# Performance work log

Measured on AMD Instinct MI355X. Metric: run time of the kernel, lower is better.

The kernel has to match this reference:

```python
import jax, jax.numpy as jnp
import numpy as np

K_CURV = 1.0   # Lorentz(k=1.0)
EPS = 1e-6


def _project(space):
    # lift space components onto hyperboloid: t = sqrt(k + ||s||^2)
    t = jnp.sqrt(K_CURV + jnp.sum(space * space, axis=-1, keepdims=True))
    return jnp.concatenate([t, space], axis=-1)


def setup_inputs():
    key = jax.random.key(0)
    B, N, D, H = 4, 1024, 128, 8
    ks = jax.random.split(key, 7)
    # valid Lorentz points: [B, N, D] with x[...,0] the time coordinate
    x = _project(jax.random.normal(ks[0], (B, N, D - 1), dtype=jnp.float32) * 0.5)
    scale = 1.0 / np.sqrt(D)
    Wq = jax.random.normal(ks[1], (H, D - 1, D), dtype=jnp.float32) * scale
    Wk = jax.random.normal(ks[2], (H, D - 1, D), dtype=jnp.float32) * scale
    Wv = jax.random.normal(ks[3], (H, D - 1, D), dtype=jnp.float32) * scale
    bq = jnp.zeros((H, D - 1), dtype=jnp.float32)
    bk = jnp.zeros((H, D - 1), dtype=jnp.float32)
    bv = jnp.zeros((H, D - 1), dtype=jnp.float32)
    beta = jnp.ones((H,), dtype=jnp.float32)
    gamma = jnp.zeros((H,), dtype=jnp.float32)
    return {"x": x, "Wq": Wq, "bq": bq, "Wk": Wk, "bk": bk, "Wv": Wv, "bv": bv,
            "beta": beta, "gamma": gamma}


def _lorentz_fc(x, W, b):
    # HyboNet-style Lorentz fully-connected (identity activation), all heads at once.
    # x: [B,N,D], W: [H,D-1,D], b: [H,D-1] -> [H,B,N,D] on the hyperboloid
    space = jnp.einsum('bnd,hed->hbne', x, W) + b[:, None, None, :]
    return _project(space)


def reference(x, Wq, bq, Wk, bk, Wv, bv, beta, gamma):
    D = x.shape[-1]
    sign = jnp.concatenate([-jnp.ones((1,), x.dtype), jnp.ones((D - 1,), x.dtype)])
    Q = _lorentz_fc(x, Wq, bq)   # [H,B,N,D]
    K = _lorentz_fc(x, Wk, bk)
    V = _lorentz_fc(x, Wv, bv)
    # pairwise Minkowski inner product <q,k>_L = -t_q t_k + s_q . s_k
    inner = jnp.einsum('hbid,hbjd->hbij', Q * sign, K)          # [H,B,N,N]
    dists = jnp.arccosh(jnp.maximum(-inner / K_CURV, 1.0 + EPS)) * np.sqrt(K_CURV)
    scores = -beta[:, None, None, None] * dists - gamma[:, None, None, None]
    attn = jax.nn.softmax(scores, axis=-1)
    # Lorentz midpoint: normalize weighted sum back onto the hyperboloid
    mid = jnp.einsum('hbij,hbjd->hbid', attn, V)                # [H,B,N,D]
    mnorm = jnp.einsum('hbid,hbid->hbi', mid * sign, mid)       # <m,m>_L (negative)
    head_out = mid * (np.sqrt(K_CURV) / jnp.sqrt(jnp.maximum(-mnorm, EPS)))[..., None]
    # direct_concat: concatenate space parts, recompute time coordinate
    H = head_out.shape[0]
    t = head_out[..., 0]                                        # [H,B,N]
    s = jnp.moveaxis(head_out[..., 1:], 0, 2)                   # [B,N,H,D-1]
    space_cat = s.reshape(s.shape[0], s.shape[1], -1)           # [B,N,H*(D-1)]
    time = jnp.sqrt(jnp.maximum(jnp.sum(t * t, axis=0) - (H - 1) * K_CURV, EPS))
    return jnp.concatenate([time[..., None], space_cat], axis=-1)  # [B,N,H*(D-1)+1]
```

## Files before the change

### kernel.cpp

```cpp
#include <hip/hip_runtime.h>

typedef __attribute__((ext_vector_type(8))) short short8_t;
typedef __attribute__((ext_vector_type(4))) short short4_t;
typedef __attribute__((ext_vector_type(4))) float float4_t;
typedef __attribute__((ext_vector_type(2))) unsigned int uint2_t;

__device__ __forceinline__ unsigned short f2bf(float f) {
    unsigned u = __builtin_bit_cast(unsigned, f);
    u += 0x7FFFu + ((u >> 16) & 1u);
    return (unsigned short)(u >> 16);
}

__device__ __forceinline__ unsigned pk_bf16(float a, float b) {
    unsigned r;
    asm("v_cvt_pk_bf16_f32 %0, %1, %2" : "=v"(r) : "v"(a), "v"(b));
    return r;
}

#define MFMA(A, B, C) __builtin_amdgcn_mfma_f32_16x16x32_bf16((A), (B), (C), 0, 0, 0)

__global__ __launch_bounds__(256) void k_proj(
    const float* __restrict__ x,
    const float* __restrict__ Wq, const float* __restrict__ bq,
    const float* __restrict__ Wk, const float* __restrict__ bk,
    const float* __restrict__ Wv, const float* __restrict__ bv,
    unsigned short* __restrict__ Qs, unsigned short* __restrict__ Kb,
    unsigned short* __restrict__ Vt)
{
    __shared__ __align__(16) unsigned char lds[17408 + 34816 + 1024];
    unsigned short* Xs  = (unsigned short*)lds;
    unsigned short* Ws  = (unsigned short*)(lds + 17408);
    float*          ssqB = (float*)(lds + 17408 + 34816);
    unsigned short* Ot  = Ws;
    unsigned short* OtT = Ws;

    const int tid = threadIdx.x;
    const int m0  = blockIdx.x * 64;
    const int h   = blockIdx.y;
    const int mat = blockIdx.z;
    const float* W  = (mat == 0) ? Wq : ((mat == 1) ? Wk : Wv);
    const float* bb = (mat == 0) ? bq : ((mat == 1) ? bk : bv);

    #pragma unroll
    for (int p = 0; p < 8; p++) {
        int r = p * 8 + (tid >> 5), c = (tid & 31) * 4;
        float4_t v = *(const float4_t*)(x + (m0 + r) * 128 + c);
        uint2_t u; u[0] = pk_bf16(v[0], v[1]); u[1] = pk_bf16(v[2], v[3]);
        *(uint2_t*)(Xs + r * 136 + c) = u;
    }
    #pragma unroll
    for (int p = 0; p < 16; p++) {
        int e = p * 8 + (tid >> 5), c = (tid & 31) * 4;
        float4_t v = {0.f, 0.f, 0.f, 0.f};
        if (e < 127) v = *(const float4_t*)(W + (h * 127 + e) * 128 + c);
        uint2_t u; u[0] = pk_bf16(v[0], v[1]); u[1] = pk_bf16(v[2], v[3]);
        *(uint2_t*)(Ws + e * 136 + c) = u;
    }
    __syncthreads();

    const int w = tid >> 6, lane = tid & 63, li = lane & 15, lg = lane >> 4;
    float4_t acc[4][2];
    #pragma unroll
    for (int i = 0; i < 4; i++)
        #pragma unroll
        for (int j = 0; j < 2; j++) acc[i][j] = (float4_t){0.f, 0.f, 0.f, 0.f};

    #pragma unroll
    for (int kk = 0; kk < 4; kk++) {
        short8_t Bf[2];
        #pragma unroll
        for (int ni = 0; ni < 2; ni++)
            Bf[ni] = *(short8_t*)(Ws + (w * 32 + ni * 16 + li) * 136 + kk * 32 + lg * 8);
        #pragma unroll
        for (int mi = 0; mi < 4; mi++) {
            short8_t A = *(short8_t*)(Xs + (mi * 16 + li) * 136 + kk * 32 + lg * 8);
            #pragma unroll
            for (int ni = 0; ni < 2; ni++) acc[mi][ni] = MFMA(A, Bf[ni], acc[mi][ni]);
        }
    }
    #pragma unroll
    for (int ni = 0; ni < 2; ni++) {
        int e = w * 32 + ni * 16 + li;
        float bvv = (e < 127) ? bb[h * 127 + e] : 0.0f;
        #pragma unroll
        for (int mi = 0; mi < 4; mi++)
            #pragma unroll
            for (int r = 0; r < 4; r++) acc[mi][ni][r] += bvv;
    }
    #pragma unroll
    for (int mi = 0; mi < 4; mi++) {
        #pragma unroll
        for (int r = 0; r < 4; r++) {
            float s = acc[mi][0][r] * acc[mi][0][r] + acc[mi][1][r] * acc[mi][1][r];
            s += __shfl_xor(s, 1);  s += __shfl_xor(s, 2);
            s += __shfl_xor(s, 4);  s += __shfl_xor(s, 8);
            if (li == 0) ssqB[(mi * 16 + lg * 4 + r) * 4 + w] = s;
        }
    }
    __syncthreads();

    if (mat < 2) {
        #pragma unroll
        for (int mi = 0; mi < 4; mi++)
            #pragma unroll
            for (int ni = 0; ni < 2; ni++) {
                int e = w * 32 + ni * 16 + li;
                if (e < 127) {
                    #pragma unroll
                    for (int r = 0; r < 4; r++)
                        Ot[(mi * 16 + lg * 4 + r) * 136 + 1 + e] = f2bf(acc[mi][ni][r]);
                }
            }
        if (tid < 64) {
            float s = ssqB[tid * 4] + ssqB[tid * 4 + 1] + ssqB[tid * 4 + 2] + ssqB[tid * 4 + 3];
            float t = sqrtf(1.0f + s);
            Ot[tid * 136] = f2bf(mat == 0 ? -t : t);
        }
        __syncthreads();
        unsigned short* dst = ((mat == 0) ? Qs : Kb) + (h * 4096 + m0) * 128;
        #pragma unroll
        for (int p = 0; p < 4; p++) {
            int r = p * 16 + (tid >> 4), c = (tid & 15) * 8;
            *(short8_t*)(dst + r * 128 + c) = *(short8_t*)(Ot + r * 136 + c);
        }
    } else {
        #pragma unroll
        for (int mi = 0; mi < 4; mi++)
            #pragma unroll
            for (int ni = 0; ni < 2; ni++) {
                int e = w * 32 + ni * 16 + li;
                if (e < 127) {
                    uint2_t u;
                    u[0] = pk_bf16(acc[mi][ni][0], acc[mi][ni][1]);
                    u[1] = pk_bf16(acc[mi][ni][2], acc[mi][ni][3]);
                    *(uint2_t*)(OtT + (1 + e) * 72 + mi * 16 + lg * 4) = u;
                }
            }
        if (tid < 64) {
            float s = ssqB[tid * 4] + ssqB[tid * 4 + 1] + ssqB[tid * 4 + 2] + ssqB[tid * 4 + 3];
            OtT[tid] = f2bf(sqrtf(1.0f + s));
        }
        __syncthreads();
        int b = m0 >> 10, n0 = m0 & 1023;
        unsigned short* dst = Vt + (h * 4 + b) * 131072 + n0;
        #pragma unroll
        for (int p = 0; p < 4; p++) {
            int d = p * 32 + (tid >> 3), nc = (tid & 7) * 8;
            *(short8_t*)(dst + d * 1024 + nc) = *(short8_t*)(OtT + d * 72 + nc);
        }
    }
}

__global__ __launch_bounds__(256) void k_attn(
    const unsigned short* __restrict__ Qsg, const unsigned short* __restrict__ Kb,
    const unsigned short* __restrict__ Vt,
    const float* __restrict__ beta, const float* __restrict__ gamma,
    float* __restrict__ out, float* __restrict__ tsq)
{
    __shared__ __align__(16) unsigned char lds[45056];
    unsigned short* Ks  = (unsigned short*)lds;
    unsigned short* Vts = (unsigned short*)(lds + 17408);
    unsigned short* Ps  = (unsigned short*)(lds + 35840);
    float*          ow  = (float*)lds;

    const int tid = threadIdx.x, w = tid >> 6, lane = tid & 63;
    const int li = lane & 15, lg = lane >> 4;

    const int bid = blockIdx.x;
    const int hb = (bid & 7) * 4 + (bid >> 7);
    const int qt = (bid >> 3) & 15;
    const int h = hb >> 2, b = hb & 3;
    const int q0 = qt * 64;

    const unsigned short* Qp = Qsg + (h * 4096 + b * 1024) * 128;
    const unsigned short* Kp = Kb  + (h * 4096 + b * 1024) * 128;
    const unsigned short* Vp = Vt  + (h * 4 + b) * 131072;
    const float bet = beta[h];
    (void)gamma;

    short8_t qf[4];
    const int qrow = q0 + w * 16 + li;
    #pragma unroll
    for (int kk = 0; kk < 4; kk++)
        qf[kk] = *(const short8_t*)(Qp + qrow * 128 + kk * 32 + lg * 8);

    float4_t amid[8];
    #pragma unroll
    for (int df = 0; df < 8; df++) amid[df] = (float4_t){0.f, 0.f, 0.f, 0.f};
    float m = -INFINITY, lsum = 0.0f;

    for (int j0 = 0; j0 < 1024; j0 += 64) {
        __syncthreads();
        #pragma unroll
        for (int p = 0; p < 4; p++) {
            int r = p * 16 + (tid >> 4), c = (tid & 15) * 8;
            *(short8_t*)(Ks + r * 136 + c) = *(const short8_t*)(Kp + (j0 + r) * 128 + c);
        }
        #pragma unroll
        for (int p = 0; p < 4; p++) {
            int d = p * 32 + (tid >> 3), c = (tid & 7) * 8;
            *(short8_t*)(Vts + d * 72 + c) = *(const short8_t*)(Vp + d * 1024 + j0 + c);
        }
        __syncthreads();

        float4_t as[4];
        #pragma unroll
        for (int jf = 0; jf < 4; jf++) as[jf] = (float4_t){0.f, 0.f, 0.f, 0.f};
        #pragma unroll
        for (int kk = 0; kk < 4; kk++) {
            #pragma unroll
            for (int jf = 0; jf < 4; jf++) {
                short8_t A = *(short8_t*)(Ks + (jf * 16 + li) * 136 + kk * 32 + lg * 8);
                as[jf] = MFMA(A, qf[kk], as[jf]);
            }
        }
        float s2[16];
        float tm = -INFINITY;
        #pragma unroll
        for (int jf = 0; jf < 4; jf++) {
            #pragma unroll
            for (int r = 0; r < 4; r++) {
                float z = fmaxf(-as[jf][r], 1.0f + 1e-6f);
                float wv = z + __builtin_amdgcn_sqrtf(__builtin_fmaf(z, z, -1.0f));
                float s = -bet * __builtin_amdgcn_logf(wv);
                s2[jf * 4 + r] = s;
                tm = fmaxf(tm, s);
            }
        }
        tm = fmaxf(tm, __shfl_xor(tm, 16));
        tm = fmaxf(tm, __shfl_xor(tm, 32));
        if (__any(tm > m + 8.0f)) {
            float mn = fmaxf(m, tm);
            float scale = __builtin_amdgcn_exp2f(m - mn);
            lsum *= scale;
            #pragma unroll
            for (int df = 0; df < 8; df++)
                #pragma unroll
                for (int r = 0; r < 4; r++) amid[df][r] *= scale;
            m = mn;
        }
        float ps_ = 0.0f;
        #pragma unroll
        for (int jf = 0; jf < 4; jf++) {
            float p0 = __builtin_amdgcn_exp2f(s2[jf * 4 + 0] - m);
            float p1 = __builtin_amdgcn_exp2f(s2[jf * 4 + 1] - m);
            float p2 = __builtin_amdgcn_exp2f(s2[jf * 4 + 2] - m);
            float p3 = __builtin_amdgcn_exp2f(s2[jf * 4 + 3] - m);
            ps_ += (p0 + p1) + (p2 + p3);
            uint2_t u; u[0] = pk_bf16(p0, p1); u[1] = pk_bf16(p2, p3);
            *(uint2_t*)(Ps + (w * 16 + li) * 72 + jf * 16 + lg * 4) = u;
        }
        ps_ += __shfl_xor(ps_, 16);
        ps_ += __shfl_xor(ps_, 32);
        lsum += ps_;
        asm volatile("s_waitcnt lgkmcnt(0)" ::: "memory");
        __builtin_amdgcn_sched_barrier(0);
        #pragma unroll
        for (int kk2 = 0; kk2 < 2; kk2++) {
            short8_t Bp = *(short8_t*)(Ps + (w * 16 + li) * 72 + kk2 * 32 + lg * 8);
            #pragma unroll
            for (int df = 0; df < 8; df++) {
                short8_t A = *(short8_t*)(Vts + (df * 16 + li) * 72 + kk2 * 32 + lg * 8);
                amid[df] = MFMA(A, Bp, amid[df]);
            }
        }
    }

    float invl = 1.0f / lsum;
    float ssq = 0.0f;
    #pragma unroll
    for (int df = 0; df < 8; df++) {
        #pragma unroll
        for (int r = 0; r < 4; r++) {
            float v = amid[df][r] * invl;
            amid[df][r] = v;
            ssq += v * v;
        }
    }
    ssq += __shfl_xor(ssq, 16);
    ssq += __shfl_xor(ssq, 32);
    float tmid = __shfl(amid[0][0], li);
    float denom = fmaxf(2.0f * tmid * tmid - ssq, 1e-6f);
    float rs = 1.0f / sqrtf(denom);

    __syncthreads();
    #pragma unroll
    for (int df = 0; df < 8; df++) {
        #pragma unroll
        for (int r = 0; r < 4; r++)
            ow[w * 2112 + li * 132 + df * 16 + lg * 4 + r] = amid[df][r] * rs;
    }
    asm volatile("s_waitcnt lgkmcnt(0)" ::: "memory");
    __builtin_amdgcn_sched_barrier(0);

    #pragma unroll
    for (int i = 0; i < 16; i++) {
        int n = q0 + w * 16 + i;
        float v0 = ow[w * 2112 + i * 132 + lane];
        float v1 = ow[w * 2112 + i * 132 + 64 + lane];
        float* orow = out + (b * 1024 + n) * 1017;
        if (lane == 0) tsq[h * 4096 + b * 1024 + n] = v0 * v0;
        else           orow[h * 127 + lane] = v0;
        orow[h * 127 + 64 + lane] = v1;
    }
}

__global__ __launch_bounds__(256) void k_time(const float* __restrict__ tsq,
                                              float* __restrict__ out)
{
    int mrow = blockIdx.x * 256 + threadIdx.x;
    float s = 0.0f;
    #pragma unroll
    for (int h = 0; h < 8; h++) s += tsq[h * 4096 + mrow];
    out[mrow * 1017] = sqrtf(fmaxf(s - 7.0f, 1e-6f));
}

extern "C" void kernel_launch(void* const* d_in, const int* in_sizes, int n_in,
                              void* d_out, int out_size, void* d_ws, size_t ws_size,
                              hipStream_t stream)
{
    const float* x    = (const float*)d_in[0];
    const float* Wq   = (const float*)d_in[1];
    const float* bq   = (const float*)d_in[2];
    const float* Wk   = (const float*)d_in[3];
    const float* bk   = (const float*)d_in[4];
    const float* Wv   = (const float*)d_in[5];
    const float* bv   = (const float*)d_in[6];
    const float* beta = (const float*)d_in[7];
    const float* gam  = (const float*)d_in[8];
    float* out = (float*)d_out;

    unsigned char* ws = (unsigned char*)d_ws;
    unsigned short* Qs = (unsigned short*)(ws);
    unsigned short* Kb = (unsigned short*)(ws + 8388608);
    unsigned short* Vt = (unsigned short*)(ws + 16777216);
    float*          ts = (float*)(ws + 25165824);

    k_proj<<<dim3(64, 8, 3), 256, 0, stream>>>(x, Wq, bq, Wk, bk, Wv, bv, Qs, Kb, Vt);
    k_attn<<<dim3(512), 256, 0, stream>>>(Qs, Kb, Vt, beta, gam, out, ts);
    k_time<<<dim3(16), 256, 0, stream>>>(ts, out);
}
```

Measured before the change: 144.2 us.

## Double-buffer K/V tiles in attention and fuse Q/K/V projections per block

The attention kernel now prefetches the next K and V tiles into registers while computing the current tile, then writes them to a second LDS buffer, so each iteration needs one barrier instead of two. It also raises wave priority around the MFMA sections. The projection kernel processes all three weight matrices in one block, reusing the converted x tile and prefetching the next weight into registers, which cuts the grid by a factor of three. The cost is higher LDS use and register pressure in both kernels, which may lower occupancy, and fewer projection blocks to spread across the GPU.

```diff
diff --git a/kernel.cpp b/kernel.cpp
--- a/kernel.cpp
+++ b/kernel.cpp
@@ -19,7 +19,7 @@
 
 #define MFMA(A, B, C) __builtin_amdgcn_mfma_f32_16x16x32_bf16((A), (B), (C), 0, 0, 0)
 
-__global__ __launch_bounds__(256) void k_proj(
+__global__ __launch_bounds__(256, 2) void k_proj(
     const float* __restrict__ x,
     const float* __restrict__ Wq, const float* __restrict__ bq,
     const float* __restrict__ Wk, const float* __restrict__ bk,
@@ -27,19 +27,15 @@
     unsigned short* __restrict__ Qs, unsigned short* __restrict__ Kb,
     unsigned short* __restrict__ Vt)
 {
-    __shared__ __align__(16) unsigned char lds[17408 + 34816 + 1024];
+    __shared__ __align__(16) unsigned char lds[71680];
     unsigned short* Xs  = (unsigned short*)lds;
     unsigned short* Ws  = (unsigned short*)(lds + 17408);
-    float*          ssqB = (float*)(lds + 17408 + 34816);
-    unsigned short* Ot  = Ws;
-    unsigned short* OtT = Ws;
+    unsigned short* Ot  = (unsigned short*)(lds + 52224);
+    float*          ssqB = (float*)(lds + 70656);
 
     const int tid = threadIdx.x;
     const int m0  = blockIdx.x * 64;
     const int h   = blockIdx.y;
-    const int mat = blockIdx.z;
-    const float* W  = (mat == 0) ? Wq : ((mat == 1) ? Wk : Wv);
-    const float* bb = (mat == 0) ? bq : ((mat == 1) ? bk : bv);
 
     #pragma unroll
     for (int p = 0; p < 8; p++) {
@@ -48,105 +44,126 @@
         uint2_t u; u[0] = pk_bf16(v[0], v[1]); u[1] = pk_bf16(v[2], v[3]);
         *(uint2_t*)(Xs + r * 136 + c) = u;
     }
+    const int we = tid >> 5, wc = (tid & 31) * 4;
+    float4_t wreg[16];
     #pragma unroll
     for (int p = 0; p < 16; p++) {
-        int e = p * 8 + (tid >> 5), c = (tid & 31) * 4;
-        float4_t v = {0.f, 0.f, 0.f, 0.f};
-        if (e < 127) v = *(const float4_t*)(W + (h * 127 + e) * 128 + c);
-        uint2_t u; u[0] = pk_bf16(v[0], v[1]); u[1] = pk_bf16(v[2], v[3]);
-        *(uint2_t*)(Ws + e * 136 + c) = u;
-    }
-    __syncthreads();
+        int e = p * 8 + we;
+        wreg[p] = (e < 127) ? *(const float4_t*)(Wq + (h * 127 + e) * 128 + wc)
+                            : (float4_t){0.f, 0.f, 0.f, 0.f};
+    }
 
     const int w = tid >> 6, lane = tid & 63, li = lane & 15, lg = lane >> 4;
-    float4_t acc[4][2];
-    #pragma unroll
-    for (int i = 0; i < 4; i++)
-        #pragma unroll
-        for (int j = 0; j < 2; j++) acc[i][j] = (float4_t){0.f, 0.f, 0.f, 0.f};
-
-    #pragma unroll
-    for (int kk = 0; kk < 4; kk++) {
-        short8_t Bf[2];
-        #pragma unroll
-        for (int ni = 0; ni < 2; ni++)
-            Bf[ni] = *(short8_t*)(Ws + (w * 32 + ni * 16 + li) * 136 + kk * 32 + lg * 8);
+
+    for (int mat = 0; mat < 3; mat++) {
+        #pragma unroll
+        for (int p = 0; p < 16; p++) {
+            int e = p * 8 + we;
+            uint2_t u; u[0] = pk_bf16(wreg[p][0], wreg[p][1]);
+                       u[1] = pk_bf16(wreg[p][2], wreg[p][3]);
+            *(uint2_t*)(Ws + e * 136 + wc) = u;
+        }
+        if (mat < 2) {
+            const float* Wn = (mat == 0) ? Wk : Wv;
+            #pragma unroll
+            for (int p = 0; p < 16; p++) {
+                int e = p * 8 + we;
+                wreg[p] = (e < 127) ? *(const float4_t*)(Wn + (h * 127 + e) * 128 + wc)
+                                    : (float4_t){0.f, 0.f, 0.f, 0.f};
+            }
+        }
+        __syncthreads();
+
+        float4_t acc[4][2];
+        #pragma unroll
+        for (int i = 0; i < 4; i++)
+            #pragma unroll
+            for (int j = 0; j < 2; j++) acc[i][j] = (float4_t){0.f, 0.f, 0.f, 0.f};
+
+        #pragma unroll
+        for (int kk = 0; kk < 4; kk++) {
+            short8_t Bf[2];
+            #pragma unroll
+            for (int ni = 0; ni < 2; ni++)
+                Bf[ni] = *(short8_t*)(Ws + (w * 32 + ni * 16 + li) * 136 + kk * 32 + lg * 8);
+            #pragma unroll
+            for (int mi = 0; mi < 4; mi++) {
+                short8_t A = *(short8_t*)(Xs + (mi * 16 + li) * 136 + kk * 32 + lg * 8);
+                #pragma unroll
+                for (int ni = 0; ni < 2; ni++) acc[mi][ni] = MFMA(A, Bf[ni], acc[mi][ni]);
+            }
+        }
+        const float* bb = (mat == 0) ? bq : ((mat == 1) ? bk : bv);
+        #pragma unroll
+        for (int ni = 0; ni < 2; ni++) {
+            int e = w * 32 + ni * 16 + li;
+            float bvv = (e < 127) ? bb[h * 127 + e] : 0.0f;
+            #pragma unroll
+            for (int mi = 0; mi < 4; mi++)
+                #pragma unroll
+                for (int r = 0; r < 4; r++) acc[mi][ni][r] += bvv;
+        }
         #pragma unroll
         for (int mi = 0; mi < 4; mi++) {
-            short8_t A = *(short8_t*)(Xs + (mi * 16 + li) * 136 + kk * 32 + lg * 8);
-            #pragma unroll
-            for (int ni = 0; ni < 2; ni++) acc[mi][ni] = MFMA(A, Bf[ni], acc[mi][ni]);
-        }
-    }
-    #pragma unroll
-    for (int ni = 0; ni < 2; ni++) {
-        int e = w * 32 + ni * 16 + li;
-        float bvv = (e < 127) ? bb[h * 127 + e] : 0.0f;
-        #pragma unroll
-        for (int mi = 0; mi < 4; mi++)
-            #pragma unroll
-            for (int r = 0; r < 4; r++) acc[mi][ni][r] += bvv;
-    }
-    #pragma unroll
-    for (int mi = 0; mi < 4; mi++) {
-        #pragma unroll
-        for (int r = 0; r < 4; r++) {
-            float s = acc[mi][0][r] * acc[mi][0][r] + acc[mi][1][r] * acc[mi][1][r];
-            s += __shfl_xor(s, 1);  s += __shfl_xor(s, 2);
-            s += __shfl_xor(s, 4);  s += __shfl_xor(s, 8);
-            if (li == 0) ssqB[(mi * 16 + lg * 4 + r) * 4 + w] = s;
-        }
-    }
-    __syncthreads();
-
-    if (mat < 2) {
-        #pragma unroll
-        for (int mi = 0; mi < 4; mi++)
-            #pragma unroll
-            for (int ni = 0; ni < 2; ni++) {
-                int e = w * 32 + ni * 16 + li;
-                if (e < 127) {
-                    #pragma unroll
-                    for (int r = 0; r < 4; r++)
-                        Ot[(mi * 16 + lg * 4 + r) * 136 + 1 + e] = f2bf(acc[mi][ni][r]);
+            #pragma unroll
+            for (int r = 0; r < 4; r++) {
+                float s = acc[mi][0][r] * acc[mi][0][r] + acc[mi][1][r] * acc[mi][1][r];
+                s += __shfl_xor(s, 1);  s += __shfl_xor(s, 2);
+                s += __shfl_xor(s, 4);  s += __shfl_xor(s, 8);
+                if (li == 0) ssqB[(mi * 16 + lg * 4 + r) * 4 + w] = s;
+            }
+        }
+        __syncthreads();
+
+        if (mat < 2) {
+            #pragma unroll
+            for (int mi = 0; mi < 4; mi++)
+                #pragma unroll
+                for (int ni = 0; ni < 2; ni++) {
+                    int e = w * 32 + ni * 16 + li;
+                    if (e < 127) {
+                        #pragma unroll
+                        for (int r = 0; r < 4; r++)
+                            Ot[(mi * 16 + lg * 4 + r) * 136 + 1 + e] = f2bf(acc[mi][ni][r]);
+                    }
                 }
-            }
-        if (tid < 64) {
-            float s = ssqB[tid * 4] + ssqB[tid * 4 + 1] + ssqB[tid * 4 + 2] + ssqB[tid * 4 + 3];
-            float t = sqrtf(1.0f + s);
-            Ot[tid * 136] = f2bf(mat == 0 ? -t : t);
-        }
-        __syncthreads();
-        unsigned short* dst = ((mat == 0) ? Qs : Kb) + (h * 4096 + m0) * 128;
-        #pragma unroll
-        for (int p = 0; p < 4; p++) {
-            int r = p * 16 + (tid >> 4), c = (tid & 15) * 8;
-            *(short8_t*)(dst + r * 128 + c) = *(short8_t*)(Ot + r * 136 + c);
-        }
-    } else {
-        #pragma unroll
-        for (int mi = 0; mi < 4; mi++)
-            #pragma unroll
-            for (int ni = 0; ni < 2; ni++) {
-                int e = w * 32 + ni * 16 + li;
-                if (e < 127) {
-                    uint2_t u;
-                    u[0] = pk_bf16(acc[mi][ni][0], acc[mi][ni][1]);
-                    u[1] = pk_bf16(acc[mi][ni][2], acc[mi][ni][3]);
-                    *(uint2_t*)(OtT + (1 + e) * 72 + mi * 16 + lg * 4) = u;
+            if (tid < 64) {
+                float s = ssqB[tid * 4] + ssqB[tid * 4 + 1] + ssqB[tid * 4 + 2] + ssqB[tid * 4 + 3];
+                float t = sqrtf(1.0f + s);
+                Ot[tid * 136] = f2bf(mat == 0 ? -t : t);
+            }
+            __syncthreads();
+            unsigned short* dst = ((mat == 0) ? Qs : Kb) + (h * 4096 + m0) * 128;
+            #pragma unroll
+            for (int p = 0; p < 4; p++) {
+                int r = p * 16 + (tid >> 4), c = (tid & 15) * 8;
+                *(short8_t*)(dst + r * 128 + c) = *(short8_t*)(Ot + r * 136 + c);
+            }
+        } else {
+            #pragma unroll
+            for (int mi = 0; mi < 4; mi++)
+                #pragma unroll
+                for (int ni = 0; ni < 2; ni++) {
+                    int e = w * 32 + ni * 16 + li;
+                    if (e < 127) {
+                        uint2_t u;
+                        u[0] = pk_bf16(acc[mi][ni][0], acc[mi][ni][1]);
+                        u[1] = pk_bf16(acc[mi][ni][2], acc[mi][ni][3]);
+                        *(uint2_t*)(Ot + (1 + e) * 72 + mi * 16 + lg * 4) = u;
+                    }
                 }
-            }
-        if (tid < 64) {
-            float s = ssqB[tid * 4] + ssqB[tid * 4 + 1] + ssqB[tid * 4 + 2] + ssqB[tid * 4 + 3];
-            OtT[tid] = f2bf(sqrtf(1.0f + s));
-        }
-        __syncthreads();
-        int b = m0 >> 10, n0 = m0 & 1023;
-        unsigned short* dst = Vt + (h * 4 + b) * 131072 + n0;
-        #pragma unroll
-        for (int p = 0; p < 4; p++) {
-            int d = p * 32 + (tid >> 3), nc = (tid & 7) * 8;
-            *(short8_t*)(dst + d * 1024 + nc) = *(short8_t*)(OtT + d * 72 + nc);
+            if (tid < 64) {
+                float s = ssqB[tid * 4] + ssqB[tid * 4 + 1] + ssqB[tid * 4 + 2] + ssqB[tid * 4 + 3];
+                Ot[tid] = f2bf(sqrtf(1.0f + s));
+            }
+            __syncthreads();
+            int b = m0 >> 10, n0 = m0 & 1023;
+            unsigned short* dst = Vt + (h * 4 + b) * 131072 + n0;
+            #pragma unroll
+            for (int p = 0; p < 4; p++) {
+                int d = p * 32 + (tid >> 3), nc = (tid & 7) * 8;
+                *(short8_t*)(dst + d * 1024 + nc) = *(short8_t*)(Ot + d * 72 + nc);
+            }
         }
     }
 }
@@ -157,11 +174,13 @@
     const float* __restrict__ beta, const float* __restrict__ gamma,
     float* __restrict__ out, float* __restrict__ tsq)
 {
-    __shared__ __align__(16) unsigned char lds[45056];
-    unsigned short* Ks  = (unsigned short*)lds;
-    unsigned short* Vts = (unsigned short*)(lds + 17408);
-    unsigned short* Ps  = (unsigned short*)(lds + 35840);
-    float*          ow  = (float*)lds;
+    __shared__ __align__(16) unsigned char lds[80896];
+    unsigned short* Kbuf0 = (unsigned short*)lds;
+    unsigned short* Kbuf1 = (unsigned short*)(lds + 17408);
+    unsigned short* Vbuf0 = (unsigned short*)(lds + 34816);
+    unsigned short* Vbuf1 = (unsigned short*)(lds + 53248);
+    unsigned short* Ps    = (unsigned short*)(lds + 71680);
+    float*          ow    = (float*)lds;
 
     const int tid = threadIdx.x, w = tid >> 6, lane = tid & 63;
     const int li = lane & 15, lg = lane >> 4;
@@ -178,6 +197,11 @@
     const float bet = beta[h];
     (void)gamma;
 
+    const int kr = tid >> 4, kc = (tid & 15) * 8;
+    const int vd = tid >> 3, vc = (tid & 7) * 8;
+    const unsigned short* Kld = Kp + kr * 128 + kc;
+    const unsigned short* Vld = Vp + vd * 1024 + vc;
+
     short8_t qf[4];
     const int qrow = q0 + w * 16 + li;
     #pragma unroll
@@ -189,31 +213,49 @@
     for (int df = 0; df < 8; df++) amid[df] = (float4_t){0.f, 0.f, 0.f, 0.f};
     float m = -INFINITY, lsum = 0.0f;
 
-    for (int j0 = 0; j0 < 1024; j0 += 64) {
-        __syncthreads();
-        #pragma unroll
-        for (int p = 0; p < 4; p++) {
-            int r = p * 16 + (tid >> 4), c = (tid & 15) * 8;
-            *(short8_t*)(Ks + r * 136 + c) = *(const short8_t*)(Kp + (j0 + r) * 128 + c);
-        }
-        #pragma unroll
-        for (int p = 0; p < 4; p++) {
-            int d = p * 32 + (tid >> 3), c = (tid & 7) * 8;
-            *(short8_t*)(Vts + d * 72 + c) = *(const short8_t*)(Vp + d * 1024 + j0 + c);
-        }
-        __syncthreads();
+    short8_t kreg[4], vreg[4];
+    #pragma unroll
+    for (int p = 0; p < 4; p++) {
+        kreg[p] = *(const short8_t*)(Kld + p * 2048);
+        vreg[p] = *(const short8_t*)(Vld + p * 32768);
+    }
+    #pragma unroll
+    for (int p = 0; p < 4; p++) {
+        *(short8_t*)(Kbuf0 + (p * 16 + kr) * 136 + kc) = kreg[p];
+        *(short8_t*)(Vbuf0 + (p * 32 + vd) * 72 + vc) = vreg[p];
+    }
+    __syncthreads();
+
+    for (int t = 0; t < 16; t++) {
+        unsigned short* Kc = (t & 1) ? Kbuf1 : Kbuf0;
+        unsigned short* Vc = (t & 1) ? Vbuf1 : Vbuf0;
+        unsigned short* Kn = (t & 1) ? Kbuf0 : Kbuf1;
+        unsigned short* Vn = (t & 1) ? Vbuf0 : Vbuf1;
+
+        if (t < 15) {
+            const int j0n = (t + 1) * 64;
+            #pragma unroll
+            for (int p = 0; p < 4; p++) {
+                kreg[p] = *(const short8_t*)(Kld + j0n * 128 + p * 2048);
+                vreg[p] = *(const short8_t*)(Vld + p * 32768 + j0n);
+            }
+        }
+        __builtin_amdgcn_sched_barrier(0);
 
         float4_t as[4];
         #pragma unroll
         for (int jf = 0; jf < 4; jf++) as[jf] = (float4_t){0.f, 0.f, 0.f, 0.f};
+        __builtin_amdgcn_s_setprio(1);
         #pragma unroll
         for (int kk = 0; kk < 4; kk++) {
             #pragma unroll
             for (int jf = 0; jf < 4; jf++) {
-                short8_t A = *(short8_t*)(Ks + (jf * 16 + li) * 136 + kk * 32 + lg * 8);
+                short8_t A = *(short8_t*)(Kc + (jf * 16 + li) * 136 + kk * 32 + lg * 8);
                 as[jf] = MFMA(A, qf[kk], as[jf]);
             }
         }
+        __builtin_amdgcn_s_setprio(0);
+
         float s2[16];
         float tm = -INFINITY;
         #pragma unroll
@@ -255,15 +297,27 @@
         lsum += ps_;
         asm volatile("s_waitcnt lgkmcnt(0)" ::: "memory");
         __builtin_amdgcn_sched_barrier(0);
+
+        __builtin_amdgcn_s_setprio(1);
         #pragma unroll
         for (int kk2 = 0; kk2 < 2; kk2++) {
             short8_t Bp = *(short8_t*)(Ps + (w * 16 + li) * 72 + kk2 * 32 + lg * 8);
             #pragma unroll
             for (int df = 0; df < 8; df++) {
-                short8_t A = *(short8_t*)(Vts + (df * 16 + li) * 72 + kk2 * 32 + lg * 8);
+                short8_t A = *(short8_t*)(Vc + (df * 16 + li) * 72 + kk2 * 32 + lg * 8);
                 amid[df] = MFMA(A, Bp, amid[df]);
             }
         }
+        __builtin_amdgcn_s_setprio(0);
+
+        if (t < 15) {
+            #pragma unroll
+            for (int p = 0; p < 4; p++) {
+                *(short8_t*)(Kn + (p * 16 + kr) * 136 + kc) = kreg[p];
+                *(short8_t*)(Vn + (p * 32 + vd) * 72 + vc) = vreg[p];
+            }
+        }
+        __syncthreads();
     }
 
     float invl = 1.0f / lsum;
@@ -283,7 +337,6 @@
     float denom = fmaxf(2.0f * tmid * tmid - ssq, 1e-6f);
     float rs = 1.0f / sqrtf(denom);
 
-    __syncthreads();
     #pragma unroll
     for (int df = 0; df < 8; df++) {
         #pragma unroll
@@ -336,7 +389,7 @@
     unsigned short* Vt = (unsigned short*)(ws + 16777216);
     float*          ts = (float*)(ws + 25165824);
 
-    k_proj<<<dim3(64, 8, 3), 256, 0, stream>>>(x, Wq, bq, Wk, bk, Wv, bv, Qs, Kb, Vt);
+    k_proj<<<dim3(64, 8), 256, 0, stream>>>(x, Wq, bq, Wk, bk, Wv, bv, Qs, Kb, Vt);
     k_attn<<<dim3(512), 256, 0, stream>>>(Qs, Kb, Vt, beta, gam, out, ts);
     k_time<<<dim3(16), 256, 0, stream>>>(ts, out);
 }
```

New measurement: 143.7 us. About the same (-0.3%).

## Split attention KV range across wave pairs and load K/V directly from global

Applied to the files above, without the earlier changes.

Each block now handles 32 queries with two waves per 16-query group, each wave processing half of the key range. The partial softmax states are merged through LDS at the end. K and V fragments are read straight from global memory instead of being staged cooperatively in LDS, which removes the per-tile block barriers. The grid doubles to 1024 blocks with a 3-blocks-per-SM occupancy hint. The cost is more redundant global and L2 traffic for K/V, an extra merge step, and half the waves sitting idle during the epilogue.

```diff
diff --git a/kernel.cpp b/kernel.cpp
--- a/kernel.cpp
+++ b/kernel.cpp
@@ -151,26 +151,27 @@
     }
 }
 
-__global__ __launch_bounds__(256) void k_attn(
+__global__ __launch_bounds__(256, 3) void k_attn(
     const unsigned short* __restrict__ Qsg, const unsigned short* __restrict__ Kb,
     const unsigned short* __restrict__ Vt,
     const float* __restrict__ beta, const float* __restrict__ gamma,
     float* __restrict__ out, float* __restrict__ tsq)
 {
-    __shared__ __align__(16) unsigned char lds[45056];
-    unsigned short* Ks  = (unsigned short*)lds;
-    unsigned short* Vts = (unsigned short*)(lds + 17408);
-    unsigned short* Ps  = (unsigned short*)(lds + 35840);
-    float*          ow  = (float*)lds;
+    __shared__ __align__(16) unsigned char lds[42752];
+    unsigned short* Ps  = (unsigned short*)lds;
+    float*          mrg = (float*)(lds + 9216);
+    float*          ow  = (float*)(lds + 25856);
 
     const int tid = threadIdx.x, w = tid >> 6, lane = tid & 63;
     const int li = lane & 15, lg = lane >> 4;
+    const int qsub = w >> 1, half = w & 1;
 
     const int bid = blockIdx.x;
-    const int hb = (bid & 7) * 4 + (bid >> 7);
-    const int qt = (bid >> 3) & 15;
+    const int g = bid >> 3;
+    const int hb = (bid & 7) + 8 * (g & 3);
+    const int qs = g >> 2;
     const int h = hb >> 2, b = hb & 3;
-    const int q0 = qt * 64;
+    const int q0 = qs * 32;
 
     const unsigned short* Qp = Qsg + (h * 4096 + b * 1024) * 128;
     const unsigned short* Kp = Kb  + (h * 4096 + b * 1024) * 128;
@@ -179,7 +180,7 @@
     (void)gamma;
 
     short8_t qf[4];
-    const int qrow = q0 + w * 16 + li;
+    const int qrow = q0 + qsub * 16 + li;
     #pragma unroll
     for (int kk = 0; kk < 4; kk++)
         qf[kk] = *(const short8_t*)(Qp + qrow * 128 + kk * 32 + lg * 8);
@@ -189,31 +190,26 @@
     for (int df = 0; df < 8; df++) amid[df] = (float4_t){0.f, 0.f, 0.f, 0.f};
     float m = -INFINITY, lsum = 0.0f;
 
-    for (int j0 = 0; j0 < 1024; j0 += 64) {
-        __syncthreads();
-        #pragma unroll
-        for (int p = 0; p < 4; p++) {
-            int r = p * 16 + (tid >> 4), c = (tid & 15) * 8;
-            *(short8_t*)(Ks + r * 136 + c) = *(const short8_t*)(Kp + (j0 + r) * 128 + c);
-        }
-        #pragma unroll
-        for (int p = 0; p < 4; p++) {
-            int d = p * 32 + (tid >> 3), c = (tid & 7) * 8;
-            *(short8_t*)(Vts + d * 72 + c) = *(const short8_t*)(Vp + d * 1024 + j0 + c);
-        }
-        __syncthreads();
+    const int j0base = half * 512;
+    for (int t = 0; t < 8; t++) {
+        const int j0 = j0base + t * 64;
 
         float4_t as[4];
         #pragma unroll
         for (int jf = 0; jf < 4; jf++) as[jf] = (float4_t){0.f, 0.f, 0.f, 0.f};
         #pragma unroll
-        for (int kk = 0; kk < 4; kk++) {
-            #pragma unroll
-            for (int jf = 0; jf < 4; jf++) {
-                short8_t A = *(short8_t*)(Ks + (jf * 16 + li) * 136 + kk * 32 + lg * 8);
-                as[jf] = MFMA(A, qf[kk], as[jf]);
-            }
-        }
+        for (int jf = 0; jf < 4; jf++) {
+            const unsigned short* kr0 = Kp + (j0 + jf * 16 + li) * 128 + lg * 8;
+            short8_t k0 = *(const short8_t*)(kr0);
+            short8_t k1 = *(const short8_t*)(kr0 + 32);
+            short8_t k2 = *(const short8_t*)(kr0 + 64);
+            short8_t k3 = *(const short8_t*)(kr0 + 96);
+            as[jf] = MFMA(k0, qf[0], as[jf]);
+            as[jf] = MFMA(k1, qf[1], as[jf]);
+            as[jf] = MFMA(k2, qf[2], as[jf]);
+            as[jf] = MFMA(k3, qf[3], as[jf]);
+        }
+
         float s2[16];
         float tm = -INFINITY;
         #pragma unroll
@@ -255,16 +251,47 @@
         lsum += ps_;
         asm volatile("s_waitcnt lgkmcnt(0)" ::: "memory");
         __builtin_amdgcn_sched_barrier(0);
+
         #pragma unroll
         for (int kk2 = 0; kk2 < 2; kk2++) {
             short8_t Bp = *(short8_t*)(Ps + (w * 16 + li) * 72 + kk2 * 32 + lg * 8);
+            const unsigned short* vr0 = Vp + li * 1024 + j0 + kk2 * 32 + lg * 8;
             #pragma unroll
             for (int df = 0; df < 8; df++) {
-                short8_t A = *(short8_t*)(Vts + (df * 16 + li) * 72 + kk2 * 32 + lg * 8);
+                short8_t A = *(const short8_t*)(vr0 + df * 16384);
                 amid[df] = MFMA(A, Bp, amid[df]);
             }
         }
     }
+
+    if (half == 1) {
+        float* mb = mrg + qsub * 2080;
+        #pragma unroll
+        for (int df = 0; df < 8; df++)
+            #pragma unroll
+            for (int r = 0; r < 4; r++)
+                mb[li * 130 + df * 16 + lg * 4 + r] = amid[df][r];
+        if (lg == 0) { mb[li * 130 + 128] = m; mb[li * 130 + 129] = lsum; }
+    }
+    __syncthreads();
+    if (half == 1) return;
+
+    {
+        float* mb = mrg + qsub * 2080;
+        float mB = mb[li * 130 + 128];
+        float lB = mb[li * 130 + 129];
+        float mN = fmaxf(m, mB);
+        float sA = __builtin_amdgcn_exp2f(m - mN);
+        float sB = __builtin_amdgcn_exp2f(mB - mN);
+        lsum = lsum * sA + lB * sB;
+        #pragma unroll
+        for (int df = 0; df < 8; df++)
+            #pragma unroll
+            for (int r = 0; r < 4; r++)
+                amid[df][r] = amid[df][r] * sA + mb[li * 130 + df * 16 + lg * 4 + r] * sB;
+    }
+    asm volatile("s_waitcnt lgkmcnt(0)" ::: "memory");
+    __builtin_amdgcn_sched_barrier(0);
 
     float invl = 1.0f / lsum;
     float ssq = 0.0f;
@@ -283,21 +310,20 @@
     float denom = fmaxf(2.0f * tmid * tmid - ssq, 1e-6f);
     float rs = 1.0f / sqrtf(denom);
 
-    __syncthreads();
     #pragma unroll
     for (int df = 0; df < 8; df++) {
         #pragma unroll
         for (int r = 0; r < 4; r++)
-            ow[w * 2112 + li * 132 + df * 16 + lg * 4 + r] = amid[df][r] * rs;
+            ow[qsub * 2112 + li * 132 + df * 16 + lg * 4 + r] = amid[df][r] * rs;
     }
     asm volatile("s_waitcnt lgkmcnt(0)" ::: "memory");
     __builtin_amdgcn_sched_barrier(0);
 
     #pragma unroll
     for (int i = 0; i < 16; i++) {
-        int n = q0 + w * 16 + i;
-        float v0 = ow[w * 2112 + i * 132 + lane];
-        float v1 = ow[w * 2112 + i * 132 + 64 + lane];
+        int n = q0 + qsub * 16 + i;
+        float v0 = ow[qsub * 2112 + i * 132 + lane];
+        float v1 = ow[qsub * 2112 + i * 132 + 64 + lane];
         float* orow = out + (b * 1024 + n) * 1017;
         if (lane == 0) tsq[h * 4096 + b * 1024 + n] = v0 * v0;
         else           orow[h * 127 + lane] = v0;
@@ -337,6 +363,6 @@
     float*          ts = (float*)(ws + 25165824);
 
     k_proj<<<dim3(64, 8, 3), 256, 0, stream>>>(x, Wq, bq, Wk, bk, Wv, bv, Qs, Kb, Vt);
-    k_attn<<<dim3(512), 256, 0, stream>>>(Qs, Kb, Vt, beta, gam, out, ts);
+    k_attn<<<dim3(1024), 256, 0, stream>>>(Qs, Kb, Vt, beta, gam, out, ts);
     k_time<<<dim3(16), 256, 0, stream>>>(ts, out);
 }
```

After: 219.0 us. +51.9%, slower.
